# Optimization experiments

Hardware: AMD Instinct MI355X
Metric: run time of the kernel (lower is better)

The kernel has to match this reference:

```python
import jax, jax.numpy as jnp
import numpy as np
from jax.scipy.special import erf

N_POINTS = 5000
N_EVENTS = 1_000_000


def setup_inputs() -> dict:
    key = jax.random.key(0)
    k1, k2, k3, k4 = jax.random.split(key, 4)
    data_idx = jax.random.randint(k1, (N_EVENTS, 2), 0, N_POINTS, dtype=jnp.int32)
    data_t = jax.random.uniform(k2, (N_EVENTS,), dtype=jnp.float32) * 10.0
    # learned parameters, matching torch.rand(...)*0.5 init
    z0 = jax.random.uniform(k3, (N_POINTS, 2), dtype=jnp.float32) * 0.5
    v0 = jax.random.uniform(k4, (N_POINTS, 2), dtype=jnp.float32) * 0.5
    beta = jnp.ones((1, 1), dtype=jnp.float32)  # beta init = 1.0
    t0 = jnp.float32(0.0)
    tn = jnp.float32(10.0)
    return {"data_idx": data_idx, "data_t": data_t, "t0": t0, "tn": tn,
            "z0": z0, "v0": v0, "beta": beta}


def reference(data_idx, data_t, t0, tn, z0, v0, beta):
    b = beta[0, 0]
    # ---- event intensity: sum over events of (beta - ||z_i(t) - z_j(t)||^2)
    i = data_idx[:, 0]
    j = data_idx[:, 1]
    dz_e = (z0[i] - z0[j]) + (v0[i] - v0[j]) * data_t[:, None]  # [E,2]
    d_event = jnp.sum(dz_e * dz_e, axis=-1)                     # [E]
    n_events = data_t.shape[0]
    event_intensity = n_events * b - jnp.sum(d_event)

    # ---- non-event intensity: analytic integral over all node pairs i<j
    n = z0.shape[0]
    pi_idx, pj_idx = jnp.triu_indices(n, k=1)  # static node-pair list
    dz = z0[pi_idx] - z0[pj_idx]  # [P,2]
    dv = v0[pi_idx] - v0[pj_idx]  # [P,2]
    a2 = jnp.sum(dz * dz, axis=-1)       # ||dz||^2
    b2 = jnp.sum(dv * dv, axis=-1)       # ||dv||^2
    ab = jnp.sum(dz * dv, axis=-1)       # dz . dv
    bnorm = jnp.sqrt(b2)
    mu = ab / b2
    # integral_{t0}^{tn} exp(beta - ||dz + dv t||^2) dt
    #   = exp(beta - a2 + ab^2/b2) * sqrt(pi)/(2|dv|) * [erf(|dv|(tn+mu)) - erf(|dv|(t0+mu))]
    pref = jnp.exp(b - a2 + ab * mu) * (jnp.sqrt(jnp.pi) / (2.0 * bnorm))
    integral = pref * (erf(bnorm * (tn + mu)) - erf(bnorm * (t0 + mu)))
    non_event_intensity = jnp.sum(integral)

    log_likelihood = event_intensity - non_event_intensity
    return log_likelihood.reshape(1, 1)
```

## Files before the change

kernel.cpp:

```cpp
#include <hip/hip_runtime.h>
#include <math.h>

#define NTHR 256
#define MAXBLK 4096


typedef float v2f __attribute__((ext_vector_type(2)));

__global__ void pack_kernel(const float* __restrict__ z0,
                            const float* __restrict__ v0,
                            float4* __restrict__ pts, int n_pts) {
    int p = blockIdx.x * blockDim.x + threadIdx.x;
    if (p < n_pts)
        pts[p] = make_float4(z0[2 * p], z0[2 * p + 1], v0[2 * p], v0[2 * p + 1]);
}

#define ERF_A1 0.0705230784f
#define ERF_A2 0.0422820123f
#define ERF_A3 0.0092705272f
#define ERF_A4 0.0001520143f
#define ERF_A5 0.0002765672f
#define ERF_A6 0.0000430638f

__device__ __forceinline__ float erf728(float x) {
    float ax = fabsf(x);
    float h = fmaf(ERF_A6, ax, ERF_A5);
    h = fmaf(h, ax, ERF_A4);
    h = fmaf(h, ax, ERF_A3);
    h = fmaf(h, ax, ERF_A2);
    h = fmaf(h, ax, ERF_A1);
    float u = fmaf(h, ax, 1.0f);
    float w = __builtin_amdgcn_rcpf(u);
    w = w * w; w = w * w; w = w * w; w = w * w;
    return copysignf(1.0f - w, x);
}

__device__ __forceinline__ v2f erf728_2(v2f x) {
    v2f ax; ax.x = fabsf(x.x); ax.y = fabsf(x.y);
    v2f h = ERF_A6 * ax + ERF_A5;
    h = h * ax + ERF_A4;
    h = h * ax + ERF_A3;
    h = h * ax + ERF_A2;
    h = h * ax + ERF_A1;
    v2f u = h * ax + 1.0f;
    v2f w; w.x = __builtin_amdgcn_rcpf(u.x); w.y = __builtin_amdgcn_rcpf(u.y);
    w = w * w; w = w * w; w = w * w; w = w * w;
    v2f e = 1.0f - w;
    e.x = copysignf(e.x, x.x);
    e.y = copysignf(e.y, x.y);
    return e;
}

__device__ __forceinline__ float pair_val(float4 Pi, float4 Pj,
                                          float b, float t0, float tn) {
    const float SPI2 = 0.88622692545275801365f;
    const float L2E  = 1.4426950408889634f;
    float dzx = Pi.x - Pj.x, dzy = Pi.y - Pj.y;
    float dvx = Pi.z - Pj.z, dvy = Pi.w - Pj.w;
    float a2 = fmaf(dzx, dzx, dzy * dzy);
    float b2 = fmaf(dvx, dvx, dvy * dvy);
    float ab = fmaf(dzx, dvx, dzy * dvy);
    float r  = __builtin_amdgcn_rsqf(b2);
    float mu = ab * (r * r);
    float e0 = fmaf(ab, mu, b - a2);
    float E  = __builtin_amdgcn_exp2f(e0 * L2E);
    float bn = b2 * r;
    float x1 = bn * (tn + mu);
    float x0 = bn * (t0 + mu);
    return (E * (SPI2 * r)) * (erf728(x1) - erf728(x0));
}

__device__ __forceinline__ v2f pair_val2(float4 Pi, float4 A, float4 B,
                                         float b, float t0, float tn) {
    const float SPI2 = 0.88622692545275801365f;
    const float L2E  = 1.4426950408889634f;
    v2f dzx = {Pi.x - A.x, Pi.x - B.x};
    v2f dzy = {Pi.y - A.y, Pi.y - B.y};
    v2f dvx = {Pi.z - A.z, Pi.z - B.z};
    v2f dvy = {Pi.w - A.w, Pi.w - B.w};
    v2f a2 = dzx * dzx + dzy * dzy;
    v2f b2 = dvx * dvx + dvy * dvy;
    v2f ab = dzx * dvx + dzy * dvy;
    v2f r;  r.x = __builtin_amdgcn_rsqf(b2.x); r.y = __builtin_amdgcn_rsqf(b2.y);
    v2f mu = ab * (r * r);
    v2f e0 = ab * mu + (b - a2);
    v2f E;  E.x = __builtin_amdgcn_exp2f(e0.x * L2E);
            E.y = __builtin_amdgcn_exp2f(e0.y * L2E);
    v2f bn = b2 * r;
    v2f x1 = bn * (tn + mu);
    v2f x0 = bn * (t0 + mu);
    v2f d = erf728_2(x1) - erf728_2(x0);
    return (E * (r * SPI2)) * d;
}

__device__ __forceinline__ float row_sweep(const float4* __restrict__ pts,
                                           float4 Pi, int jstart, int n_pts,
                                           float b, float t0, float tn) {
    v2f acc = {0.f, 0.f};
    int j = jstart + threadIdx.x;
    for (; j + NTHR < n_pts; j += 2 * NTHR) {
        float4 Pj0 = pts[j];
        float4 Pj1 = pts[j + NTHR];
        acc += pair_val2(Pi, Pj0, Pj1, b, t0, tn);
    }
    float a = acc.x + acc.y;
    if (j < n_pts)
        a += pair_val(Pi, pts[j], b, t0, tn);
    return a;
}

__device__ __forceinline__ float event_sum(const int2* __restrict__ idx,
                                           const float* __restrict__ t,
                                           const float4* __restrict__ pts,
                                           int n_events, int nblocks) {
    const int4*   idx4 = (const int4*)idx;
    const float2* t2   = (const float2*)t;
    const int half = n_events >> 1;
    float acc = 0.0f;
    for (int h = blockIdx.x * NTHR + threadIdx.x; h < half;
         h += nblocks * NTHR) {
        int4 ij = idx4[h];
        float2 tt = t2[h];
        float4 pi0 = pts[ij.x], pj0 = pts[ij.y];
        float4 pi1 = pts[ij.z], pj1 = pts[ij.w];
        float dx0 = (pi0.x - pj0.x) + (pi0.z - pj0.z) * tt.x;
        float dy0 = (pi0.y - pj0.y) + (pi0.w - pj0.w) * tt.x;
        float dx1 = (pi1.x - pj1.x) + (pi1.z - pj1.z) * tt.y;
        float dy1 = (pi1.y - pj1.y) + (pi1.w - pj1.w) * tt.y;
        acc = fmaf(dx0, dx0, fmaf(dy0, dy0, acc));
        acc = fmaf(dx1, dx1, fmaf(dy1, dy1, acc));
    }
    if ((n_events & 1) && blockIdx.x == 0 && threadIdx.x == 0) {
        int e = n_events - 1;
        int2 ij = idx[e];
        float te = t[e];
        float4 pi = pts[ij.x], pj = pts[ij.y];
        float dx = (pi.x - pj.x) + (pi.z - pj.z) * te;
        float dy = (pi.y - pj.y) + (pi.w - pj.w) * te;
        acc = fmaf(dx, dx, fmaf(dy, dy, acc));
    }
    return acc;
}

__device__ __forceinline__ float pair_sum(const float4* __restrict__ pts,
                                          int n_pts, float b, float t0,
                                          float tn) {
    const int n_rows = n_pts - 1;
    const int r1 = blockIdx.x;
    float acc = 0.0f;
    if (r1 < n_rows) {
        const int r2 = n_rows - 1 - r1;
        float4 Pi1 = pts[r1];
        acc += row_sweep(pts, Pi1, r1 + 1, n_pts, b, t0, tn);
        if (r2 > r1) {
            float4 Pi2 = pts[r2];
            acc += row_sweep(pts, Pi2, r2 + 1, n_pts, b, t0, tn);
        }
    }
    return acc;
}

__global__ __launch_bounds__(NTHR) void cvm_main_kernel(
    const int2* __restrict__ idx, const float* __restrict__ t,
    const float4* __restrict__ pts,
    const float* __restrict__ t0p, const float* __restrict__ tnp,
    const float* __restrict__ betap,
    int n_events, int n_pts, double* __restrict__ partials) {

    const float b  = betap[0];
    const float t0 = t0p[0];
    const float tn = tnp[0];
    const int nblocks = gridDim.x;

    float accf;
    if (blockIdx.x & 1) {
        accf = pair_sum(pts, n_pts, b, t0, tn);
        accf += event_sum(idx, t, pts, n_events, nblocks);
    } else {
        accf = event_sum(idx, t, pts, n_events, nblocks);
        accf += pair_sum(pts, n_pts, b, t0, tn);
    }

    double v = (double)accf;
    #pragma unroll
    for (int off = 32; off > 0; off >>= 1) v += __shfl_down(v, off, 64);
    __shared__ double wsum[4];
    if ((threadIdx.x & 63) == 0) wsum[threadIdx.x >> 6] = v;
    __syncthreads();
    if (threadIdx.x == 0)
        partials[blockIdx.x] = wsum[0] + wsum[1] + wsum[2] + wsum[3];
}

__global__ void finish_kernel(const double* __restrict__ partials, int nblk,
                              const float* __restrict__ betap,
                              float* __restrict__ out, int n_events) {
    double v = 0.0;
    for (int i = threadIdx.x; i < nblk; i += NTHR) v += partials[i];
    #pragma unroll
    for (int off = 32; off > 0; off >>= 1) v += __shfl_down(v, off, 64);
    __shared__ double wsum[4];
    if ((threadIdx.x & 63) == 0) wsum[threadIdx.x >> 6] = v;
    __syncthreads();
    if (threadIdx.x == 0)
        out[0] = (float)((double)n_events * (double)betap[0] -
                         (wsum[0] + wsum[1] + wsum[2] + wsum[3]));
}

extern "C" void kernel_launch(void* const* d_in, const int* in_sizes, int n_in,
                              void* d_out, int out_size, void* d_ws, size_t ws_size,
                              hipStream_t stream) {
    const int2*  idx  = (const int2*)d_in[0];
    const float* t    = (const float*)d_in[1];
    const float* t0   = (const float*)d_in[2];
    const float* tn   = (const float*)d_in[3];
    const float* z0   = (const float*)d_in[4];
    const float* v0   = (const float*)d_in[5];
    const float* beta = (const float*)d_in[6];
    const int n_events = in_sizes[1];
    const int n_pts    = in_sizes[4] / 2;

    double* partials = (double*)d_ws;
    float4* pts = (float4*)((char*)d_ws + MAXBLK * sizeof(double));

    const int n_rows = n_pts - 1;
    int nblk = (n_rows + 1) / 2;
    if (nblk < 1) nblk = 1;
    if (nblk > MAXBLK) nblk = MAXBLK;

    pack_kernel<<<(n_pts + NTHR - 1) / NTHR, NTHR, 0, stream>>>(z0, v0, pts, n_pts);
    cvm_main_kernel<<<nblk, NTHR, 0, stream>>>(idx, t, pts, t0, tn, beta,
                                               n_events, n_pts, partials);
    finish_kernel<<<1, NTHR, 0, stream>>>(partials, nblk, beta,
                                          (float*)d_out, n_events);
}
```

Baseline: 96.61 us.

## Use SoA point arrays with paired loads and share one reciprocal across erfs

The pack kernel now also writes the point data as four separate arrays (x, y, vx, vy). The pair loop reads two adjacent points per thread as 2-wide vector loads, and handles one leading pair separately to keep those loads aligned. In the erf evaluation, the two reciprocals of u1 and u0 are replaced by a single reciprocal of their product, which saves a transcendental per pair at the cost of extra multiplies and some overflow risk. An odd point count would read one element past the valid data into the padding.

```diff
diff --git a/kernel.cpp b/kernel.cpp
--- a/kernel.cpp
+++ b/kernel.cpp
@@ -3,16 +3,23 @@
 
 #define NTHR 256
 #define MAXBLK 4096
+#define PTS_PAD 20480
 
 
 typedef float v2f __attribute__((ext_vector_type(2)));
 
 __global__ void pack_kernel(const float* __restrict__ z0,
                             const float* __restrict__ v0,
+                            float* __restrict__ xs, float* __restrict__ ys,
+                            float* __restrict__ vxs, float* __restrict__ vys,
                             float4* __restrict__ pts, int n_pts) {
     int p = blockIdx.x * blockDim.x + threadIdx.x;
-    if (p < n_pts)
-        pts[p] = make_float4(z0[2 * p], z0[2 * p + 1], v0[2 * p], v0[2 * p + 1]);
+    if (p < n_pts) {
+        float zx = z0[2 * p], zy = z0[2 * p + 1];
+        float vx = v0[2 * p], vy = v0[2 * p + 1];
+        xs[p] = zx; ys[p] = zy; vxs[p] = vx; vys[p] = vy;
+        pts[p] = make_float4(zx, zy, vx, vy);
+    }
 }
 
 #define ERF_A1 0.0705230784f
@@ -33,22 +40,6 @@
     float w = __builtin_amdgcn_rcpf(u);
     w = w * w; w = w * w; w = w * w; w = w * w;
     return copysignf(1.0f - w, x);
-}
-
-__device__ __forceinline__ v2f erf728_2(v2f x) {
-    v2f ax; ax.x = fabsf(x.x); ax.y = fabsf(x.y);
-    v2f h = ERF_A6 * ax + ERF_A5;
-    h = h * ax + ERF_A4;
-    h = h * ax + ERF_A3;
-    h = h * ax + ERF_A2;
-    h = h * ax + ERF_A1;
-    v2f u = h * ax + 1.0f;
-    v2f w; w.x = __builtin_amdgcn_rcpf(u.x); w.y = __builtin_amdgcn_rcpf(u.y);
-    w = w * w; w = w * w; w = w * w; w = w * w;
-    v2f e = 1.0f - w;
-    e.x = copysignf(e.x, x.x);
-    e.y = copysignf(e.y, x.y);
-    return e;
 }
 
 __device__ __forceinline__ float pair_val(float4 Pi, float4 Pj,
@@ -70,14 +61,22 @@
     return (E * (SPI2 * r)) * (erf728(x1) - erf728(x0));
 }
 
-__device__ __forceinline__ v2f pair_val2(float4 Pi, float4 A, float4 B,
-                                         float b, float t0, float tn) {
+__device__ __forceinline__ v2f erf_u2(v2f ax) {
+    v2f h = ERF_A6 * ax + ERF_A5;
+    h = h * ax + ERF_A4;
+    h = h * ax + ERF_A3;
+    h = h * ax + ERF_A2;
+    h = h * ax + ERF_A1;
+    return h * ax + 1.0f;
+}
+
+__device__ __forceinline__ v2f pair_val2(float Pix, float Piy, float Pivx,
+                                         float Pivy, v2f xj, v2f yj, v2f vxj,
+                                         v2f vyj, float b, float t0, float tn) {
     const float SPI2 = 0.88622692545275801365f;
     const float L2E  = 1.4426950408889634f;
-    v2f dzx = {Pi.x - A.x, Pi.x - B.x};
-    v2f dzy = {Pi.y - A.y, Pi.y - B.y};
-    v2f dvx = {Pi.z - A.z, Pi.z - B.z};
-    v2f dvy = {Pi.w - A.w, Pi.w - B.w};
+    v2f dzx = Pix - xj, dzy = Piy - yj;
+    v2f dvx = Pivx - vxj, dvy = Pivy - vyj;
     v2f a2 = dzx * dzx + dzy * dzy;
     v2f b2 = dvx * dvx + dvy * dvy;
     v2f ab = dzx * dvx + dzy * dvy;
@@ -89,24 +88,47 @@
     v2f bn = b2 * r;
     v2f x1 = bn * (tn + mu);
     v2f x0 = bn * (t0 + mu);
-    v2f d = erf728_2(x1) - erf728_2(x0);
-    return (E * (r * SPI2)) * d;
-}
-
-__device__ __forceinline__ float row_sweep(const float4* __restrict__ pts,
-                                           float4 Pi, int jstart, int n_pts,
+    v2f ax1; ax1.x = fabsf(x1.x); ax1.y = fabsf(x1.y);
+    v2f ax0; ax0.x = fabsf(x0.x); ax0.y = fabsf(x0.y);
+    v2f u1 = erf_u2(ax1);
+    v2f u0 = erf_u2(ax0);
+    v2f p = u1 * u0;
+    v2f rp; rp.x = __builtin_amdgcn_rcpf(p.x); rp.y = __builtin_amdgcn_rcpf(p.y);
+    v2f w1 = u0 * rp;
+    v2f w0 = u1 * rp;
+    w1 = w1 * w1; w1 = w1 * w1; w1 = w1 * w1; w1 = w1 * w1;
+    w0 = w0 * w0; w0 = w0 * w0; w0 = w0 * w0; w0 = w0 * w0;
+    v2f e1 = 1.0f - w1;
+    v2f e0f = 1.0f - w0;
+    e1.x = copysignf(e1.x, x1.x);  e1.y = copysignf(e1.y, x1.y);
+    e0f.x = copysignf(e0f.x, x0.x); e0f.y = copysignf(e0f.y, x0.y);
+    return (E * (r * SPI2)) * (e1 - e0f);
+}
+
+__device__ __forceinline__ float row_sweep(const float* __restrict__ xs,
+                                           const float* __restrict__ ys,
+                                           const float* __restrict__ vxs,
+                                           const float* __restrict__ vys,
+                                           const float4* __restrict__ pts,
+                                           int r, int n_pts,
                                            float b, float t0, float tn) {
+    float4 Pi = pts[r];
+    float head = 0.0f;
+    int base = r + 1;
+    if (base & 1) {
+        if (threadIdx.x == 0)
+            head = pair_val(Pi, pts[base], b, t0, tn);
+        ++base;
+    }
     v2f acc = {0.f, 0.f};
-    int j = jstart + threadIdx.x;
-    for (; j + NTHR < n_pts; j += 2 * NTHR) {
-        float4 Pj0 = pts[j];
-        float4 Pj1 = pts[j + NTHR];
-        acc += pair_val2(Pi, Pj0, Pj1, b, t0, tn);
-    }
-    float a = acc.x + acc.y;
-    if (j < n_pts)
-        a += pair_val(Pi, pts[j], b, t0, tn);
-    return a;
+    for (int jb = base + 2 * (int)threadIdx.x; jb < n_pts; jb += 2 * NTHR) {
+        v2f xj  = *(const v2f*)(xs + jb);
+        v2f yj  = *(const v2f*)(ys + jb);
+        v2f vxj = *(const v2f*)(vxs + jb);
+        v2f vyj = *(const v2f*)(vys + jb);
+        acc += pair_val2(Pi.x, Pi.y, Pi.z, Pi.w, xj, yj, vxj, vyj, b, t0, tn);
+    }
+    return head + acc.x + acc.y;
 }
 
 __device__ __forceinline__ float event_sum(const int2* __restrict__ idx,
@@ -142,7 +164,11 @@
     return acc;
 }
 
-__device__ __forceinline__ float pair_sum(const float4* __restrict__ pts,
+__device__ __forceinline__ float pair_sum(const float* __restrict__ xs,
+                                          const float* __restrict__ ys,
+                                          const float* __restrict__ vxs,
+                                          const float* __restrict__ vys,
+                                          const float4* __restrict__ pts,
                                           int n_pts, float b, float t0,
                                           float tn) {
     const int n_rows = n_pts - 1;
@@ -150,18 +176,17 @@
     float acc = 0.0f;
     if (r1 < n_rows) {
         const int r2 = n_rows - 1 - r1;
-        float4 Pi1 = pts[r1];
-        acc += row_sweep(pts, Pi1, r1 + 1, n_pts, b, t0, tn);
-        if (r2 > r1) {
-            float4 Pi2 = pts[r2];
-            acc += row_sweep(pts, Pi2, r2 + 1, n_pts, b, t0, tn);
-        }
+        acc += row_sweep(xs, ys, vxs, vys, pts, r1, n_pts, b, t0, tn);
+        if (r2 > r1)
+            acc += row_sweep(xs, ys, vxs, vys, pts, r2, n_pts, b, t0, tn);
     }
     return acc;
 }
 
 __global__ __launch_bounds__(NTHR) void cvm_main_kernel(
     const int2* __restrict__ idx, const float* __restrict__ t,
+    const float* __restrict__ xs, const float* __restrict__ ys,
+    const float* __restrict__ vxs, const float* __restrict__ vys,
     const float4* __restrict__ pts,
     const float* __restrict__ t0p, const float* __restrict__ tnp,
     const float* __restrict__ betap,
@@ -174,11 +199,11 @@
 
     float accf;
     if (blockIdx.x & 1) {
-        accf = pair_sum(pts, n_pts, b, t0, tn);
+        accf = pair_sum(xs, ys, vxs, vys, pts, n_pts, b, t0, tn);
         accf += event_sum(idx, t, pts, n_events, nblocks);
     } else {
         accf = event_sum(idx, t, pts, n_events, nblocks);
-        accf += pair_sum(pts, n_pts, b, t0, tn);
+        accf += pair_sum(xs, ys, vxs, vys, pts, n_pts, b, t0, tn);
     }
 
     double v = (double)accf;
@@ -219,17 +244,24 @@
     const int n_events = in_sizes[1];
     const int n_pts    = in_sizes[4] / 2;
 
-    double* partials = (double*)d_ws;
-    float4* pts = (float4*)((char*)d_ws + MAXBLK * sizeof(double));
+    char* base = (char*)d_ws;
+    double* partials = (double*)base;
+    float* xs  = (float*)(base + 32768);
+    float* ys  = (float*)(base + 32768 + PTS_PAD);
+    float* vxs = (float*)(base + 32768 + 2 * PTS_PAD);
+    float* vys = (float*)(base + 32768 + 3 * PTS_PAD);
+    float4* pts = (float4*)(base + 32768 + 4 * PTS_PAD);
 
     const int n_rows = n_pts - 1;
     int nblk = (n_rows + 1) / 2;
     if (nblk < 1) nblk = 1;
     if (nblk > MAXBLK) nblk = MAXBLK;
 
-    pack_kernel<<<(n_pts + NTHR - 1) / NTHR, NTHR, 0, stream>>>(z0, v0, pts, n_pts);
-    cvm_main_kernel<<<nblk, NTHR, 0, stream>>>(idx, t, pts, t0, tn, beta,
-                                               n_events, n_pts, partials);
+    pack_kernel<<<(n_pts + NTHR - 1) / NTHR, NTHR, 0, stream>>>(
+        z0, v0, xs, ys, vxs, vys, pts, n_pts);
+    cvm_main_kernel<<<nblk, NTHR, 0, stream>>>(idx, t, xs, ys, vxs, vys, pts,
+                                               t0, tn, beta, n_events, n_pts,
+                                               partials);
     finish_kernel<<<1, NTHR, 0, stream>>>(partials, nblk, beta,
                                           (float*)d_out, n_events);
 }
```

Result: no change. 96.53 us (-0.1%).
